# Performance work log

Measured on AMD Instinct MI355X. Metric: run time of the kernel, lower is better.

The kernel has to match this reference:

```python
import jax, jax.numpy as jnp
import numpy as np

QK_K = 256      # super-block size
N_SUB = 8       # sub-blocks per super-block
SUB_SIZE = QK_K // N_SUB  # 32
NMAX_4BIT = 15.0


def _quantize_scales_6bit(scales):
    # scales: (B, N_SUB). Quantize to 6-bit grid [0..63] and dequantize; STE for grads.
    s_min = scales.min(axis=-1, keepdims=True)
    s_max = scales.max(axis=-1, keepdims=True)
    s_range = jnp.maximum(s_max - s_min, 1e-8)
    s_int = jnp.clip(jnp.round((scales - s_min) / s_range * 63.0), 0.0, 63.0)
    s_dequant = s_int / 63.0 * s_range + s_min
    return scales + jax.lax.stop_gradient(s_dequant - scales)


def fake_quantize_q4_k_m(weight):
    orig_shape = weight.shape
    w = weight.reshape(-1)
    pad = (-w.size) % QK_K
    if pad:
        w = jnp.concatenate([w, jnp.zeros((pad,), dtype=w.dtype)])
    # (n_blocks, N_SUB, SUB_SIZE)
    w_sub = w.reshape(-1, N_SUB, SUB_SIZE)
    sub_min = jnp.minimum(w_sub.min(axis=-1), 0.0)   # clamp(max=0)
    sub_max = jnpum if False else jnp.maximum(w_sub.max(axis=-1), 0.0)  # clamp(min=0)
    scale_raw = jnp.maximum(sub_max - sub_min, 1e-8) / NMAX_4BIT
    scale = _quantize_scales_6bit(scale_raw)         # (n_blocks, N_SUB)
    # super-block min, rounded through fp16 with STE
    super_min_raw = sub_min.min(axis=-1, keepdims=True)  # (n_blocks, 1)
    super_min_f16 = super_min_raw.astype(jnp.float16).astype(w.dtype)
    super_min = super_min_raw + jax.lax.stop_gradient(super_min_f16 - super_min_raw)
    adj_min = sub_min - super_min                    # (n_blocks, N_SUB)
    scale_bc = jnp.maximum(scale, 1e-8)[..., None]   # (n_blocks, N_SUB, 1)
    w_int = (w_sub - super_min[..., None] - adj_min[..., None]) / scale_bc
    w_int = jnp.clip(jnp.round(w_int), 0.0, NMAX_4BIT)
    w_dequant = w_int * scale_bc + adj_min[..., None] + super_min[..., None]
    w_out = w_sub + jax.lax.stop_gradient(w_dequant - w_sub)  # STE
    w_flat = w_out.reshape(-1)
    if pad:
        w_flat = w_flat[:-pad]
    return w_flat.reshape(orig_shape)


def setup_inputs() -> dict:
    key = jax.random.key(0)
    k1, k2, k3 = jax.random.split(key, 3)
    x = jax.random.normal(k1, (2, 2048, 4096), dtype=jnp.float32)
    weight = jax.random.normal(k2, (4096, 4096), dtype=jnp.float32) * 0.02
    bias = jax.random.normal(k3, (4096,), dtype=jnp.float32)
    return {"x": x, "weight": weight, "bias": bias}


def reference(x, weight, bias):
    # _qmode = True path: fake-quantize weight to Q4_K_M grid, then dense linear.
    fq_weight = fake_quantize_q4_k_m(weight)
    return jnp.einsum('bsd,od->bso', x, fq_weight) + bias
```

## Files before the change

kernel.cpp:

```cpp
#include <hip/hip_runtime.h>
#include <hip/hip_bf16.h>
#include <hip/hip_fp16.h>


typedef __attribute__((ext_vector_type(8))) short bf16x8;
typedef __attribute__((ext_vector_type(8))) unsigned short ushort8;
typedef __attribute__((ext_vector_type(4))) float f32x4;

__device__ __forceinline__ unsigned short f2bf(float f) {
  unsigned int u = __float_as_uint(f);
  u += 0x7fffu + ((u >> 16) & 1u);
  return (unsigned short)(u >> 16);
}

__global__ __launch_bounds__(256) void prep_kernel(
    const float* __restrict__ x, unsigned short* __restrict__ xb,
    const float* __restrict__ w, unsigned short* __restrict__ wq,
    int castBlocks) {
  if ((int)blockIdx.x < castBlocks) {
    const size_t i = ((size_t)blockIdx.x * 256 + threadIdx.x) * 8;
    const float4 a = *(const float4*)(x + i);
    const float4 b = *(const float4*)(x + i + 4);
    ushort8 o = {f2bf(a.x), f2bf(a.y), f2bf(a.z), f2bf(a.w),
                 f2bf(b.x), f2bf(b.y), f2bf(b.z), f2bf(b.w)};
    *(ushort8*)(xb + i) = o;
    return;
  }
  const int qb   = blockIdx.x - castBlocks;
  const int lane = threadIdx.x & 63;
  const int wv   = threadIdx.x >> 6;
  const size_t base = (((size_t)qb * 4 + wv) * 256) + (size_t)lane * 4;
  const float4 v = *(const float4*)(w + base);

  float mn = fminf(fminf(v.x, v.y), fminf(v.z, v.w));
  float mx = fmaxf(fmaxf(v.x, v.y), fmaxf(v.z, v.w));
#pragma unroll
  for (int off = 1; off <= 4; off <<= 1) {
    mn = fminf(mn, __shfl_xor(mn, off));
    mx = fmaxf(mx, __shfl_xor(mx, off));
  }
  const float sub_min = fminf(mn, 0.0f);
  const float sub_max = fmaxf(mx, 0.0f);
  const float scale_raw = fmaxf(sub_max - sub_min, 1e-8f) / 15.0f;

  float smn = scale_raw, smx = scale_raw, supermin = sub_min;
#pragma unroll
  for (int off = 8; off <= 32; off <<= 1) {
    smn = fminf(smn, __shfl_xor(smn, off));
    smx = fmaxf(smx, __shfl_xor(smx, off));
    supermin = fminf(supermin, __shfl_xor(supermin, off));
  }
  const float s_range = fmaxf(smx - smn, 1e-8f);
  float s_int = rintf((scale_raw - smn) / s_range * 63.0f);
  s_int = fminf(fmaxf(s_int, 0.0f), 63.0f);
  float scale = s_int / 63.0f * s_range + smn;
  scale = fmaxf(scale, 1e-8f);
  const float inv_scale = 1.0f / scale;

  const float sm  = __half2float(__float2half(supermin));
  const float adj = sub_min - sm;

  float e[4] = {v.x, v.y, v.z, v.w};
  ushort4 o;
  unsigned short* op = (unsigned short*)&o;
#pragma unroll
  for (int k = 0; k < 4; ++k) {
    const float t = (e[k] - sm) - adj;
    float qv = rintf(t * inv_scale);
    qv = fminf(fmaxf(qv, 0.0f), 15.0f);
    op[k] = f2bf((qv * scale + adj) + sm);
  }
  *(ushort4*)(wq + base) = o;
}

#define BM 256
#define BN 128
#define BK 64

__device__ __forceinline__ void async_cp16(void* lds, const void* g) {
  __builtin_amdgcn_global_load_lds(
      (__attribute__((address_space(1))) void*)(void*)g,
      (__attribute__((address_space(3))) void*)lds, 16, 0, 0);
}

__global__ __launch_bounds__(256, 2) void gemm_bt_kernel(
    const unsigned short* __restrict__ A,
    const unsigned short* __restrict__ B,
    const float* __restrict__ bias,
    float* __restrict__ C,
    int M, int N, int K) {
  __shared__ unsigned short lds_a[BM * BK];
  __shared__ unsigned short lds_b[BN * BK];

  const int tid  = threadIdx.x;
  const int lane = tid & 63;
  const int wv   = tid >> 6;
  const int wm   = wv >> 1;
  const int wn   = wv & 1;
  const int bx   = blockIdx.x;
  const int by   = blockIdx.y;

  const int rloc = tid >> 3;
  const int csw  = (tid & 7) ^ (rloc & 7);
  const int koff = csw * 8;

  const unsigned short* gA[8];
  const unsigned short* gB[4];
#pragma unroll
  for (int j = 0; j < 8; ++j)
    gA[j] = A + (size_t)(by * BM + j * 32 + rloc) * K + koff;
#pragma unroll
  for (int j = 0; j < 4; ++j)
    gB[j] = B + (size_t)(bx * BN + j * 32 + rloc) * K + koff;

  f32x4 acc[8][4] = {};

  const int arow   = wm * 128 + (lane & 15);
  const int brow   = wn * 64 + (lane & 15);
  const int kslot0 = (((lane >> 4) ^ (lane & 7))) * 8;
  const int kslot1 = kslot0 ^ 32;

  for (int k0 = 0; k0 < K; k0 += BK) {
#pragma unroll
    for (int j = 0; j < 8; ++j)
      async_cp16(lds_a + j * 2048 + tid * 8, gA[j] + k0);
#pragma unroll
    for (int j = 0; j < 4; ++j)
      async_cp16(lds_b + j * 2048 + tid * 8, gB[j] + k0);
    __syncthreads();

#pragma unroll
    for (int h = 0; h < 2; ++h) {
      const int ks = h ? kslot1 : kslot0;
      bf16x8 af[8], bfr[4];
#pragma unroll
      for (int i = 0; i < 8; ++i)
        af[i] = *(const bf16x8*)(lds_a + (arow + i * 16) * BK + ks);
#pragma unroll
      for (int j = 0; j < 4; ++j)
        bfr[j] = *(const bf16x8*)(lds_b + (brow + j * 16) * BK + ks);

#pragma unroll
      for (int i = 0; i < 8; ++i)
#pragma unroll
        for (int j = 0; j < 4; ++j)
          acc[i][j] = __builtin_amdgcn_mfma_f32_16x16x32_bf16(af[i], bfr[j],
                                                              acc[i][j], 0, 0, 0);
    }
    __syncthreads();
  }

  const int rbase = by * BM + wm * 128 + (lane >> 4) * 4;
  const int cbase = bx * BN + wn * 64 + (lane & 15);
#pragma unroll
  for (int j = 0; j < 4; ++j) {
    const int c = cbase + j * 16;
    const float bv = bias[c];
#pragma unroll
    for (int i = 0; i < 8; ++i) {
#pragma unroll
      for (int r = 0; r < 4; ++r) {
        C[(size_t)(rbase + i * 16 + r) * N + c] = acc[i][j][r] + bv;
      }
    }
  }
}

extern "C" void kernel_launch(void* const* d_in, const int* in_sizes, int n_in,
                              void* d_out, int out_size, void* d_ws, size_t ws_size,
                              hipStream_t stream) {
  const float* x    = (const float*)d_in[0];
  const float* w    = (const float*)d_in[1];
  const float* bias = (const float*)d_in[2];
  float* out = (float*)d_out;

  const long long xn = in_sizes[0];
  const long long wn = in_sizes[1];
  const int N = in_sizes[2];
  const int K = (int)(wn / N);
  const int M = (int)(xn / K);

  unsigned short* xb = (unsigned short*)d_ws;
  unsigned short* wb = xb + (size_t)M * K;

  const int castBlocks  = (int)(xn / (256 * 8));
  const int quantBlocks = (int)(wn / (256 * 4));
  prep_kernel<<<castBlocks + quantBlocks, 256, 0, stream>>>(x, xb, w, wb,
                                                            castBlocks);
  gemm_bt_kernel<<<dim3(N / BN, M / BM), 256, 0, stream>>>(xb, wb, bias, out,
                                                           M, N, K);
}
```

Baseline: 287.3 us.

## Pipeline GEMM with 4-stage LDS ring, 256x256 tiles and 8 waves

Reworks the bf16 GEMM to use 256x256 output tiles with 512 threads (8 waves) and a 4-deep ring of K=32 LDS buffers. Global-to-LDS loads for stage s+3 are issued between the compute phases, and waits use explicit vmcnt/lgkmcnt counts, barriers and setprio. The aim is to hide global load latency behind MFMA work and to raise data reuse per tile. In exchange it uses more LDS per block (64 KB), so occupancy may fall, and the hand-tuned waitcnt logic is fragile.

```diff
diff --git a/kernel.cpp b/kernel.cpp
--- a/kernel.cpp
+++ b/kernel.cpp
@@ -74,8 +74,10 @@
 }
 
 #define BM 256
-#define BN 128
-#define BK 64
+#define BN 256
+#define BKS 32
+#define ABUF 8192
+#define BBUF 8192
 
 __device__ __forceinline__ void async_cp16(void* lds, const void* g) {
   __builtin_amdgcn_global_load_lds(
@@ -83,75 +85,114 @@
       (__attribute__((address_space(3))) void*)lds, 16, 0, 0);
 }
 
-__global__ __launch_bounds__(256, 2) void gemm_bt_kernel(
+__global__ __launch_bounds__(512, 2) void gemm_bt_kernel(
     const unsigned short* __restrict__ A,
     const unsigned short* __restrict__ B,
     const float* __restrict__ bias,
     float* __restrict__ C,
     int M, int N, int K) {
-  __shared__ unsigned short lds_a[BM * BK];
-  __shared__ unsigned short lds_b[BN * BK];
+  __shared__ unsigned short lds_a[4 * ABUF];
+  __shared__ unsigned short lds_b[4 * BBUF];
 
   const int tid  = threadIdx.x;
   const int lane = tid & 63;
   const int wv   = tid >> 6;
-  const int wm   = wv >> 1;
-  const int wn   = wv & 1;
+  const int wm   = wv >> 2;
+  const int wn   = wv & 3;
   const int bx   = blockIdx.x;
   const int by   = blockIdx.y;
 
-  const int rloc = tid >> 3;
-  const int csw  = (tid & 7) ^ (rloc & 7);
-  const int koff = csw * 8;
-
-  const unsigned short* gA[8];
-  const unsigned short* gB[4];
-#pragma unroll
-  for (int j = 0; j < 8; ++j)
-    gA[j] = A + (size_t)(by * BM + j * 32 + rloc) * K + koff;
-#pragma unroll
-  for (int j = 0; j < 4; ++j)
-    gB[j] = B + (size_t)(bx * BN + j * 32 + rloc) * K + koff;
+  const int rloc = tid >> 2;
+  const int cch  = (tid & 3) ^ ((rloc >> 1) & 3);
+  const int koff = cch * 8;
+
+  const unsigned short* gA0 = A + (size_t)(by * BM + rloc) * K + koff;
+  const unsigned short* gA1 = gA0 + (size_t)128 * K;
+  const unsigned short* gB0 = B + (size_t)(bx * BN + rloc) * K + koff;
+  const unsigned short* gB1 = gB0 + (size_t)128 * K;
+
+  const int m16 = lane & 15;
+  const int q   = lane >> 4;
+  const int sw  = (m16 >> 1) & 3;
+  const int ks  = ((q ^ sw) << 3);
+  const int aoff = (wm * 128 + m16) * BKS + ks;
+  const int boff = (wn * 64  + m16) * BKS + ks;
 
   f32x4 acc[8][4] = {};
 
-  const int arow   = wm * 128 + (lane & 15);
-  const int brow   = wn * 64 + (lane & 15);
-  const int kslot0 = (((lane >> 4) ^ (lane & 7))) * 8;
-  const int kslot1 = kslot0 ^ 32;
-
-  for (int k0 = 0; k0 < K; k0 += BK) {
-#pragma unroll
-    for (int j = 0; j < 8; ++j)
-      async_cp16(lds_a + j * 2048 + tid * 8, gA[j] + k0);
+  const int nsub = K / BKS;
+
+#pragma unroll
+  for (int p = 0; p < 3; ++p) {
+    const int kof = p * BKS;
+    unsigned short* la = lds_a + p * ABUF;
+    unsigned short* lb = lds_b + p * BBUF;
+    async_cp16(la + tid * 8,        gA0 + kof);
+    async_cp16(la + 4096 + tid * 8, gA1 + kof);
+    async_cp16(lb + tid * 8,        gB0 + kof);
+    async_cp16(lb + 4096 + tid * 8, gB1 + kof);
+  }
+  asm volatile("s_waitcnt vmcnt(8)" ::: "memory");
+  __builtin_amdgcn_s_barrier();
+  __builtin_amdgcn_sched_barrier(0);
+
+  for (int s = 0; s < nsub; ++s) {
+    const unsigned short* abuf = lds_a + (s & 3) * ABUF;
+    const unsigned short* bbuf = lds_b + (s & 3) * BBUF;
+    unsigned short* la = lds_a + ((s + 3) & 3) * ABUF;
+    unsigned short* lb = lds_b + ((s + 3) & 3) * BBUF;
+    const int sp  = (s + 3 < nsub) ? (s + 3) : (nsub - 1);
+    const int kof = sp * BKS;
+
+    bf16x8 af[4], bfr[4];
+#pragma unroll
+    for (int i = 0; i < 4; ++i)
+      af[i] = *(const bf16x8*)(abuf + aoff + i * (16 * BKS));
 #pragma unroll
     for (int j = 0; j < 4; ++j)
-      async_cp16(lds_b + j * 2048 + tid * 8, gB[j] + k0);
-    __syncthreads();
-
-#pragma unroll
-    for (int h = 0; h < 2; ++h) {
-      const int ks = h ? kslot1 : kslot0;
-      bf16x8 af[8], bfr[4];
-#pragma unroll
-      for (int i = 0; i < 8; ++i)
-        af[i] = *(const bf16x8*)(lds_a + (arow + i * 16) * BK + ks);
+      bfr[j] = *(const bf16x8*)(bbuf + boff + j * (16 * BKS));
+    async_cp16(la + tid * 8,        gA0 + kof);
+    async_cp16(la + 4096 + tid * 8, gA1 + kof);
+    __builtin_amdgcn_s_barrier();
+    __builtin_amdgcn_sched_barrier(0);
+    asm volatile("s_waitcnt lgkmcnt(0)" ::: "memory");
+    __builtin_amdgcn_sched_barrier(0);
+    __builtin_amdgcn_s_setprio(1);
+#pragma unroll
+    for (int i = 0; i < 4; ++i)
 #pragma unroll
       for (int j = 0; j < 4; ++j)
-        bfr[j] = *(const bf16x8*)(lds_b + (brow + j * 16) * BK + ks);
-
-#pragma unroll
-      for (int i = 0; i < 8; ++i)
-#pragma unroll
-        for (int j = 0; j < 4; ++j)
-          acc[i][j] = __builtin_amdgcn_mfma_f32_16x16x32_bf16(af[i], bfr[j],
-                                                              acc[i][j], 0, 0, 0);
-    }
-    __syncthreads();
+        acc[i][j] = __builtin_amdgcn_mfma_f32_16x16x32_bf16(af[i], bfr[j],
+                                                            acc[i][j], 0, 0, 0);
+    __builtin_amdgcn_s_setprio(0);
+    __builtin_amdgcn_s_barrier();
+    __builtin_amdgcn_sched_barrier(0);
+
+    bf16x8 ag[4];
+#pragma unroll
+    for (int i = 0; i < 4; ++i)
+      ag[i] = *(const bf16x8*)(abuf + aoff + (i + 4) * (16 * BKS));
+    async_cp16(lb + tid * 8,        gB0 + kof);
+    async_cp16(lb + 4096 + tid * 8, gB1 + kof);
+    __builtin_amdgcn_s_barrier();
+    __builtin_amdgcn_sched_barrier(0);
+    asm volatile("s_waitcnt lgkmcnt(0)" ::: "memory");
+    __builtin_amdgcn_sched_barrier(0);
+    __builtin_amdgcn_s_setprio(1);
+#pragma unroll
+    for (int i = 0; i < 4; ++i)
+#pragma unroll
+      for (int j = 0; j < 4; ++j)
+        acc[i + 4][j] = __builtin_amdgcn_mfma_f32_16x16x32_bf16(ag[i], bfr[j],
+                                                                acc[i + 4][j], 0, 0, 0);
+    __builtin_amdgcn_s_setprio(0);
+    asm volatile("s_waitcnt vmcnt(8)" ::: "memory");
+    __builtin_amdgcn_s_barrier();
+    __builtin_amdgcn_sched_barrier(0);
   }
 
   const int rbase = by * BM + wm * 128 + (lane >> 4) * 4;
-  const int cbase = bx * BN + wn * 64 + (lane & 15);
+  const int cbase = bx * BN + wn * 64 + m16;
 #pragma unroll
   for (int j = 0; j < 4; ++j) {
     const int c = cbase + j * 16;
@@ -187,6 +228,6 @@
   const int quantBlocks = (int)(wn / (256 * 4));
   prep_kernel<<<castBlocks + quantBlocks, 256, 0, stream>>>(x, xb, w, wb,
                                                             castBlocks);
-  gemm_bt_kernel<<<dim3(N / BN, M / BM), 256, 0, stream>>>(xb, wb, bias, out,
+  gemm_bt_kernel<<<dim3(N / BN, M / BM), 512, 0, stream>>>(xb, wb, bias, out,
                                                            M, N, K);
 }
```

Measured after the change: 329.7 us. +14.8%, slower.

## Triple-buffer GEMM LDS stages with async prefetch and single barrier per step

Applied to the files above, without the earlier changes.

Replaces the single-buffered BK=64 main loop with a three-stage ring of BK=32 LDS buffers. Global-to-LDS loads for two steps ahead are issued before computing the current step, with a vmcnt wait and one barrier per step instead of two syncthreads. It also raises wave priority around the MFMA block and uses a new swizzle for the narrower rows. Costs are more LDS per block and more barriers per unit of K work.

```diff
diff --git a/kernel.cpp b/kernel.cpp
--- a/kernel.cpp
+++ b/kernel.cpp
@@ -75,7 +75,9 @@
 
 #define BM 256
 #define BN 128
-#define BK 64
+#define BKS 32
+#define ABUF 8192
+#define BBUF 4096
 
 __device__ __forceinline__ void async_cp16(void* lds, const void* g) {
   __builtin_amdgcn_global_load_lds(
@@ -89,8 +91,8 @@
     const float* __restrict__ bias,
     float* __restrict__ C,
     int M, int N, int K) {
-  __shared__ unsigned short lds_a[BM * BK];
-  __shared__ unsigned short lds_b[BN * BK];
+  __shared__ unsigned short lds_a[3 * ABUF];
+  __shared__ unsigned short lds_b[3 * BBUF];
 
   const int tid  = threadIdx.x;
   const int lane = tid & 63;
@@ -100,58 +102,84 @@
   const int bx   = blockIdx.x;
   const int by   = blockIdx.y;
 
-  const int rloc = tid >> 3;
-  const int csw  = (tid & 7) ^ (rloc & 7);
-  const int koff = csw * 8;
-
-  const unsigned short* gA[8];
-  const unsigned short* gB[4];
-#pragma unroll
-  for (int j = 0; j < 8; ++j)
-    gA[j] = A + (size_t)(by * BM + j * 32 + rloc) * K + koff;
+  const int rr   = tid >> 2;
+  const int cch  = (tid & 3) ^ ((tid >> 3) & 3);
+  const int koff = cch * 8;
+
+  const unsigned short* gA[4];
+  const unsigned short* gB[2];
 #pragma unroll
   for (int j = 0; j < 4; ++j)
-    gB[j] = B + (size_t)(bx * BN + j * 32 + rloc) * K + koff;
+    gA[j] = A + (size_t)(by * BM + j * 64 + rr) * K + koff;
+#pragma unroll
+  for (int j = 0; j < 2; ++j)
+    gB[j] = B + (size_t)(bx * BN + j * 64 + rr) * K + koff;
+
+  const int m16 = lane & 15;
+  const int q   = lane >> 4;
+  const int sw  = (m16 >> 1) & 3;
+  const int ks  = ((q ^ sw) << 3);
+  const int aoff = (wm * 128 + m16) * BKS + ks;
+  const int boff = (wn * 64  + m16) * BKS + ks;
 
   f32x4 acc[8][4] = {};
 
-  const int arow   = wm * 128 + (lane & 15);
-  const int brow   = wn * 64 + (lane & 15);
-  const int kslot0 = (((lane >> 4) ^ (lane & 7))) * 8;
-  const int kslot1 = kslot0 ^ 32;
-
-  for (int k0 = 0; k0 < K; k0 += BK) {
-#pragma unroll
-    for (int j = 0; j < 8; ++j)
-      async_cp16(lds_a + j * 2048 + tid * 8, gA[j] + k0);
+  const int nsub = K / BKS;
+
+#pragma unroll
+  for (int p = 0; p < 2; ++p) {
+    unsigned short* la = lds_a + p * ABUF;
+    unsigned short* lb = lds_b + p * BBUF;
+    const int kof = p * BKS;
+#pragma unroll
+    for (int j = 0; j < 4; ++j) async_cp16(la + j * 2048 + tid * 8, gA[j] + kof);
+#pragma unroll
+    for (int j = 0; j < 2; ++j) async_cp16(lb + j * 2048 + tid * 8, gB[j] + kof);
+  }
+  asm volatile("s_waitcnt vmcnt(6)" ::: "memory");
+  __builtin_amdgcn_s_barrier();
+
+  int rb = 0;
+  int wr = 2;
+  for (int s = 0; s < nsub; ++s) {
+    const unsigned short* abuf = lds_a + rb * ABUF;
+    const unsigned short* bbuf = lds_b + rb * BBUF;
+    unsigned short* la = lds_a + wr * ABUF;
+    unsigned short* lb = lds_b + wr * BBUF;
+    const int sp  = (s + 2 < nsub) ? (s + 2) : (nsub - 1);
+    const int kof = sp * BKS;
+
+#pragma unroll
+    for (int j = 0; j < 4; ++j) async_cp16(la + j * 2048 + tid * 8, gA[j] + kof);
+#pragma unroll
+    for (int j = 0; j < 2; ++j) async_cp16(lb + j * 2048 + tid * 8, gB[j] + kof);
+
+    bf16x8 af[8], bfr[4];
+#pragma unroll
+    for (int i = 0; i < 8; ++i)
+      af[i] = *(const bf16x8*)(abuf + aoff + i * (16 * BKS));
 #pragma unroll
     for (int j = 0; j < 4; ++j)
-      async_cp16(lds_b + j * 2048 + tid * 8, gB[j] + k0);
-    __syncthreads();
-
-#pragma unroll
-    for (int h = 0; h < 2; ++h) {
-      const int ks = h ? kslot1 : kslot0;
-      bf16x8 af[8], bfr[4];
-#pragma unroll
-      for (int i = 0; i < 8; ++i)
-        af[i] = *(const bf16x8*)(lds_a + (arow + i * 16) * BK + ks);
+      bfr[j] = *(const bf16x8*)(bbuf + boff + j * (16 * BKS));
+
+    __builtin_amdgcn_s_setprio(1);
+#pragma unroll
+    for (int i = 0; i < 8; ++i)
 #pragma unroll
       for (int j = 0; j < 4; ++j)
-        bfr[j] = *(const bf16x8*)(lds_b + (brow + j * 16) * BK + ks);
-
-#pragma unroll
-      for (int i = 0; i < 8; ++i)
-#pragma unroll
-        for (int j = 0; j < 4; ++j)
-          acc[i][j] = __builtin_amdgcn_mfma_f32_16x16x32_bf16(af[i], bfr[j],
-                                                              acc[i][j], 0, 0, 0);
-    }
-    __syncthreads();
+        acc[i][j] = __builtin_amdgcn_mfma_f32_16x16x32_bf16(af[i], bfr[j],
+                                                            acc[i][j], 0, 0, 0);
+    __builtin_amdgcn_s_setprio(0);
+
+    asm volatile("s_waitcnt vmcnt(6)" ::: "memory");
+    __builtin_amdgcn_s_barrier();
+
+    rb = (rb == 2) ? 0 : rb + 1;
+    wr = (wr == 2) ? 0 : wr + 1;
   }
 
   const int rbase = by * BM + wm * 128 + (lane >> 4) * 4;
-  const int cbase = bx * BN + wn * 64 + (lane & 15);
+  const int cbase = bx * BN + wn * 64 + m16;
 #pragma unroll
   for (int j = 0; j < 4; ++j) {
     const int c = cbase + j * 16;
```

Result: slower. 308.9 us (+7.5%).

## Switch GEMM to 32x32x16 MFMA with k-sliced LDS layout

Applied to the files above, without the earlier changes.

Replaces the 16x16x32 bf16 MFMA tiles with 32x32x16 MFMA. Each wave now computes 4x2 tiles of 32x32 instead of 8x4 tiles of 16x16. The LDS layout changes from a swizzled row-major 64-wide tile to k-slices of 16 elements, with one 16-byte chunk per row per slice. The aim is fewer MFMA instructions per K step and fewer LDS fragment loads. The new layout drops the XOR swizzle and uses a 64-byte row stride within each slice, which may introduce LDS bank conflicts.

```diff
diff --git a/kernel.cpp b/kernel.cpp
--- a/kernel.cpp
+++ b/kernel.cpp
@@ -5,7 +5,7 @@
 
 typedef __attribute__((ext_vector_type(8))) short bf16x8;
 typedef __attribute__((ext_vector_type(8))) unsigned short ushort8;
-typedef __attribute__((ext_vector_type(4))) float f32x4;
+typedef __attribute__((ext_vector_type(16))) float f32x16;
 
 __device__ __forceinline__ unsigned short f2bf(float f) {
   unsigned int u = __float_as_uint(f);
@@ -100,67 +100,67 @@
   const int bx   = blockIdx.x;
   const int by   = blockIdx.y;
 
-  const int rloc = tid >> 3;
-  const int csw  = (tid & 7) ^ (rloc & 7);
-  const int koff = csw * 8;
+  const int srow  = tid >> 1;
+  const int skoff = (tid & 1) * 8;
+  const unsigned short* gA0 = A + (size_t)(by * BM + srow) * K + skoff;
+  const unsigned short* gA1 = gA0 + (size_t)128 * K;
+  const unsigned short* gB0 = B + (size_t)(bx * BN + srow) * K + skoff;
 
-  const unsigned short* gA[8];
-  const unsigned short* gB[4];
-#pragma unroll
-  for (int j = 0; j < 8; ++j)
-    gA[j] = A + (size_t)(by * BM + j * 32 + rloc) * K + koff;
-#pragma unroll
-  for (int j = 0; j < 4; ++j)
-    gB[j] = B + (size_t)(bx * BN + j * 32 + rloc) * K + koff;
+  const int r32   = lane & 31;
+  const int khalf = (lane >> 5) * 16;
+  const int abase = (wm * 128 + r32) * 32 + khalf;
+  const int bbase = (wn * 64  + r32) * 32 + khalf;
 
-  f32x4 acc[8][4] = {};
-
-  const int arow   = wm * 128 + (lane & 15);
-  const int brow   = wn * 64 + (lane & 15);
-  const int kslot0 = (((lane >> 4) ^ (lane & 7))) * 8;
-  const int kslot1 = kslot0 ^ 32;
+  f32x16 acc[4][2] = {};
 
   for (int k0 = 0; k0 < K; k0 += BK) {
 #pragma unroll
-    for (int j = 0; j < 8; ++j)
-      async_cp16(lds_a + j * 2048 + tid * 8, gA[j] + k0);
+    for (int j = 0; j < 8; ++j) {
+      const unsigned short* src = (j & 1) ? gA1 : gA0;
+      async_cp16((char*)lds_a + j * 4096 + tid * 16, src + k0 + (j >> 1) * 16);
+    }
 #pragma unroll
     for (int j = 0; j < 4; ++j)
-      async_cp16(lds_b + j * 2048 + tid * 8, gB[j] + k0);
+      async_cp16((char*)lds_b + j * 4096 + tid * 16, gB0 + k0 + j * 16);
     __syncthreads();
 
 #pragma unroll
     for (int h = 0; h < 2; ++h) {
-      const int ks = h ? kslot1 : kslot0;
-      bf16x8 af[8], bfr[4];
+      bf16x8 af[4][2], bfr[2][2];
 #pragma unroll
-      for (int i = 0; i < 8; ++i)
-        af[i] = *(const bf16x8*)(lds_a + (arow + i * 16) * BK + ks);
+      for (int t2 = 0; t2 < 2; ++t2) {
+        const int t = 2 * h + t2;
 #pragma unroll
-      for (int j = 0; j < 4; ++j)
-        bfr[j] = *(const bf16x8*)(lds_b + (brow + j * 16) * BK + ks);
-
+        for (int i = 0; i < 4; ++i)
+          af[i][t2] = *(const bf16x8*)((const char*)lds_a + t * 8192 + abase + i * 1024);
 #pragma unroll
-      for (int i = 0; i < 8; ++i)
+        for (int j = 0; j < 2; ++j)
+          bfr[j][t2] = *(const bf16x8*)((const char*)lds_b + t * 4096 + bbase + j * 1024);
+      }
 #pragma unroll
-        for (int j = 0; j < 4; ++j)
-          acc[i][j] = __builtin_amdgcn_mfma_f32_16x16x32_bf16(af[i], bfr[j],
-                                                              acc[i][j], 0, 0, 0);
+      for (int i = 0; i < 4; ++i)
+#pragma unroll
+        for (int j = 0; j < 2; ++j)
+#pragma unroll
+          for (int t2 = 0; t2 < 2; ++t2)
+            acc[i][j] = __builtin_amdgcn_mfma_f32_32x32x16_bf16(
+                af[i][t2], bfr[j][t2], acc[i][j], 0, 0, 0);
     }
     __syncthreads();
   }
 
-  const int rbase = by * BM + wm * 128 + (lane >> 4) * 4;
-  const int cbase = bx * BN + wn * 64 + (lane & 15);
+  const int rbase = by * BM + wm * 128 + 4 * (lane >> 5);
+  const int cbase = bx * BN + wn * 64 + r32;
 #pragma unroll
-  for (int j = 0; j < 4; ++j) {
-    const int c = cbase + j * 16;
+  for (int j = 0; j < 2; ++j) {
+    const int c = cbase + j * 32;
     const float bv = bias[c];
 #pragma unroll
-    for (int i = 0; i < 8; ++i) {
+    for (int i = 0; i < 4; ++i) {
 #pragma unroll
-      for (int r = 0; r < 4; ++r) {
-        C[(size_t)(rbase + i * 16 + r) * N + c] = acc[i][j][r] + bv;
+      for (int r = 0; r < 16; ++r) {
+        const int row = rbase + i * 32 + (r & 3) + 8 * (r >> 2);
+        C[(size_t)row * N + c] = acc[i][j][r] + bv;
       }
     }
   }
```

After: 320.2 us. 1.11x slower.
